# Performance work log

Measured on AMD Instinct MI355X. Metric: run time of the kernel, lower is better.

The kernel has to match this reference:

```python
import jax, jax.numpy as jnp
import numpy as np

N_NODES = 50000
N_EDGES = 800000
N_FEAT = 128
HIDDEN = 128
N_GRAPHS = 256


def gcn_conv(x, W, b, src, dst, n_nodes):
    # PyG GCNConv, add_self_loops=False, edge_weight=1:
    # out_i = sum_{(j->i)} d_j^{-1/2} d_i^{-1/2} (x_j @ W) + b, deg over target idx
    h = x @ W                                    # [N, out]
    deg = jax.ops.segment_sum(jnp.ones((src.shape[0],), h.dtype), dst,
                              num_segments=n_nodes)          # [N]
    dis = jnp.where(deg > 0, jax.lax.rsqrt(jnp.maximum(deg, 1.0)), 0.0)
    norm = dis[src] * dis[dst]                   # [E]
    msg = h[src] * norm[:, None]                 # [E, out] gather + scale
    out = jax.ops.segment_sum(msg, dst, num_segments=n_nodes)  # scatter-add
    return out + b


def setup_inputs() -> dict:
    key = jax.random.key(0)
    ks = jax.random.split(key, 12)
    x = jax.random.normal(ks[0], (N_NODES, N_FEAT), jnp.float32)
    edge_index = jax.random.randint(ks[1], (2, N_EDGES), 0, N_NODES, jnp.int64)
    batch = jnp.sort(jax.random.randint(ks[2], (N_NODES,), 0, N_GRAPHS, jnp.int64))

    def glorot(k, shape):
        lim = float(np.sqrt(6.0 / (shape[0] + shape[1])))
        return jax.random.uniform(k, shape, jnp.float32, -lim, lim)

    W1 = glorot(ks[3], (N_FEAT, HIDDEN)); b1 = jnp.zeros((HIDDEN,), jnp.float32)
    W2 = glorot(ks[4], (HIDDEN, HIDDEN)); b2 = jnp.zeros((HIDDEN,), jnp.float32)
    Wf1 = glorot(ks[5], (HIDDEN, HIDDEN // 2)); bf1 = jnp.zeros((HIDDEN // 2,), jnp.float32)
    Wl = glorot(ks[6], (HIDDEN // 2, 2)); bl = jnp.zeros((2,), jnp.float32)
    return {"x": x, "edge_index": edge_index, "batch": batch,
            "W1": W1, "b1": b1, "W2": W2, "b2": b2,
            "Wf1": Wf1, "bf1": bf1, "Wl": Wl, "bl": bl}


def reference(x, edge_index, batch, W1, b1, W2, b2, Wf1, bf1, Wl, bl):
    src, dst = edge_index[0], edge_index[1]
    h = jax.nn.relu(gcn_conv(x, W1, b1, src, dst, N_NODES))
    h = jax.nn.relu(gcn_conv(h, W2, b2, src, dst, N_NODES))
    h = gcn_conv(h, W2, b2, src, dst, N_NODES)   # conv2 applied a second time (same weights)
    # global_mean_pool over graphs
    sums = jax.ops.segment_sum(h, batch, num_segments=N_GRAPHS)      # [G, H]
    cnts = jax.ops.segment_sum(jnp.ones((h.shape[0],), h.dtype), batch,
                               num_segments=N_GRAPHS)                # [G]
    g = sums / jnp.maximum(cnts, 1.0)[:, None]
    g = jax.nn.relu(g @ Wf1 + bf1)
    logits = g @ Wl + bl
    return jax.nn.softmax(logits, axis=1)
```

## Files before the change

kernel.cpp:

```cpp
#include <hip/hip_runtime.h>
#include <hip/hip_bf16.h>

#define N_NODES 50000
#define N_EDGES 800000
#define NF 128
#define NG 256
#define CAP 64
#define NSEG 256
#define SEGE (N_EDGES / NSEG)
#define NPAD 50048
#define NPREPB 16

typedef unsigned short ushort_t;
typedef unsigned char uchar_t;
typedef __attribute__((ext_vector_type(8))) short bf16x8;
typedef __attribute__((ext_vector_type(4))) float f32x4;

__device__ __forceinline__ float b2f(ushort_t u) {
    union { unsigned i; float f; } x; x.i = ((unsigned)u) << 16; return x.f;
}
__device__ __forceinline__ ushort_t f2b(float f) {
    union { float f; unsigned i; } x; x.f = f;
    unsigned r = (x.i + 0x7fffu + ((x.i >> 16) & 1u)) >> 16;
    return (ushort_t)r;
}

__global__ __launch_bounds__(512) void k_seg_count(
        const int* __restrict__ dst, uchar_t* __restrict__ segcnt,
        float* __restrict__ gsum) {
    __shared__ unsigned int cntw[NPAD / 4];
    int tid = threadIdx.x;
    int b = blockIdx.x;
    if (b < 16) {
        ((float4*)gsum)[b * 512 + tid] = make_float4(0.f, 0.f, 0.f, 0.f);
    }
    for (int i = tid; i < NPAD / 4; i += 512) cntw[i] = 0;
    __syncthreads();
    const int* d0 = dst + b * SEGE;
    for (int e = tid; e < SEGE; e += 512) {
        int d = d0[e];
        atomicAdd(&cntw[d >> 2], 1u << ((d & 3) * 8));
    }
    __syncthreads();
    unsigned int* outw = (unsigned int*)(segcnt + (size_t)b * NPAD);
    for (int i = tid; i < NPAD / 4; i += 512) outw[i] = cntw[i];
}

__global__ void k_seg_scan(const uchar_t* __restrict__ segcnt,
                           uchar_t* __restrict__ segbase,
                           int* __restrict__ deg, float* __restrict__ dis) {
    int node = blockIdx.x * 256 + threadIdx.x;
    if (node >= N_NODES) return;
    int run = 0;
#pragma unroll 8
    for (int s = 0; s < NSEG; ++s) {
        size_t idx = (size_t)s * NPAD + node;
        int c = segcnt[idx];
        segbase[idx] = (uchar_t)min(run, 255);
        run += c;
    }
    deg[node] = min(run, CAP);
    dis[node] = (run > 0) ? rsqrtf((float)run) : 0.f;
}

__global__ __launch_bounds__(512) void k_seg_fill(
        const int* __restrict__ src, const int* __restrict__ dst,
        const uchar_t* __restrict__ segbase, ushort_t* __restrict__ csr_pad,
        const float* __restrict__ W1, const float* __restrict__ W2,
        ushort_t* __restrict__ W1h, ushort_t* __restrict__ W1l,
        ushort_t* __restrict__ W2h, ushort_t* __restrict__ W2l) {
    __shared__ unsigned int cntw[NPAD / 4];
    int tid = threadIdx.x;
    int b = blockIdx.x;
    if (b >= NSEG) {
        int base = (b - NSEG) * 2048 + tid * 4;
#pragma unroll
        for (int i = 0; i < 4; ++i) {
            int id = base + i;
            int which = id >> 14;
            int u = id & 16383;
            int k = u >> 7, c = u & 127;
            const float* W = which ? W2 : W1;
            ushort_t* Wh = which ? W2h : W1h;
            ushort_t* Wl = which ? W2l : W1l;
            float w = W[k * 128 + c];
            ushort_t hi = f2b(w);
            ushort_t lo = f2b(w - b2f(hi));
            Wh[c * 128 + k] = hi;
            Wl[c * 128 + k] = lo;
        }
        return;
    }
    for (int i = tid; i < NPAD / 4; i += 512) cntw[i] = 0;
    __syncthreads();
    const int* d0 = dst + b * SEGE;
    const int* s0 = src + b * SEGE;
    const uchar_t* brow = segbase + (size_t)b * NPAD;
    for (int e = tid; e < SEGE; e += 512) {
        int d = d0[e];
        int sh = (d & 3) * 8;
        unsigned old = atomicAdd(&cntw[d >> 2], 1u << sh);
        int pos = (old >> sh) & 0xFF;
        int slot = brow[d] + pos;
        if (slot < CAP) csr_pad[(size_t)d * CAP + slot] = (ushort_t)s0[e];
    }
}

__global__ __launch_bounds__(256) void k_gemm_mfma_f32(
        const float* __restrict__ Xf,
        const ushort_t* __restrict__ Wt_hi, const ushort_t* __restrict__ Wt_lo,
        const float* __restrict__ dis, ushort_t* __restrict__ Yb, int n) {
    __shared__ ushort_t Wlds[2][16384];
    int t = threadIdx.x;
    {
        const int4* gh = (const int4*)Wt_hi;
        const int4* gl = (const int4*)Wt_lo;
        int4* sh = (int4*)&Wlds[0][0];
        int4* sl = (int4*)&Wlds[1][0];
#pragma unroll
        for (int i = 0; i < 8; ++i) {
            int u = t + i * 256;
            int swz = u ^ ((u >> 4) & 7);
            sh[swz] = gh[u];
            sl[swz] = gl[u];
        }
    }
    __syncthreads();

    int wid = t >> 6;
    int l   = t & 63;
    int la  = l & 15;
    int kb  = l >> 4;
    int r0  = blockIdx.x * 64 + wid * 16;

    bf16x8 a[4];
    {
        int ra = min(r0 + la, n - 1);
        const float* xrow = Xf + (size_t)ra * 128 + kb * 8;
#pragma unroll
        for (int kt = 0; kt < 4; ++kt) {
            float4 v0 = *(const float4*)(xrow + kt * 32);
            float4 v1 = *(const float4*)(xrow + kt * 32 + 4);
            bf16x8 av;
            av[0] = (short)f2b(v0.x); av[1] = (short)f2b(v0.y);
            av[2] = (short)f2b(v0.z); av[3] = (short)f2b(v0.w);
            av[4] = (short)f2b(v1.x); av[5] = (short)f2b(v1.y);
            av[6] = (short)f2b(v1.z); av[7] = (short)f2b(v1.w);
            a[kt] = av;
        }
    }

    f32x4 acc[8];
#pragma unroll
    for (int ct = 0; ct < 8; ++ct) acc[ct] = (f32x4){0.f, 0.f, 0.f, 0.f};

#pragma unroll
    for (int ct = 0; ct < 8; ++ct) {
        int c = ct * 16 + la;
        int ubase = c * 128 + kb * 8;
        int sw = (c & 7) << 3;
#pragma unroll
        for (int kt = 0; kt < 4; ++kt) {
            int u16 = (ubase + kt * 32) ^ sw;
            bf16x8 bh = *(const bf16x8*)&Wlds[0][u16];
            bf16x8 bl = *(const bf16x8*)&Wlds[1][u16];
            acc[ct] = __builtin_amdgcn_mfma_f32_16x16x32_bf16(a[kt], bh, acc[ct], 0, 0, 0);
            acc[ct] = __builtin_amdgcn_mfma_f32_16x16x32_bf16(a[kt], bl, acc[ct], 0, 0, 0);
        }
    }

    float dsc[4];
#pragma unroll
    for (int j = 0; j < 4; ++j)
        dsc[j] = dis[min(r0 + kb * 4 + j, n - 1)];

    __syncthreads();
    ushort_t* tile = ((ushort_t*)Wlds) + wid * 2048;
#pragma unroll
    for (int ct = 0; ct < 8; ++ct) {
        int cc = ct * 16 + la;
#pragma unroll
        for (int j = 0; j < 4; ++j)
            tile[(kb * 4 + j) * 128 + cc] = f2b(acc[ct][j] * dsc[j]);
    }
    __syncthreads();
    {
        const int4* t4 = (const int4*)tile;
        int4* dst4 = (int4*)(Yb + (size_t)r0 * 128);
#pragma unroll
        for (int i = 0; i < 4; ++i) {
            int u = l * 4 + i;
            int row = u >> 4;
            if (r0 + row < n) dst4[u] = t4[u];
        }
    }
}

__global__ __launch_bounds__(256) void k_gemm_mfma_bf16(
        const ushort_t* __restrict__ Xb,
        const ushort_t* __restrict__ Wt_hi, const ushort_t* __restrict__ Wt_lo,
        const float* __restrict__ dis, ushort_t* __restrict__ Yb, int n) {
    __shared__ ushort_t Wlds[2][16384];
    int t = threadIdx.x;
    {
        const int4* gh = (const int4*)Wt_hi;
        const int4* gl = (const int4*)Wt_lo;
        int4* sh = (int4*)&Wlds[0][0];
        int4* sl = (int4*)&Wlds[1][0];
#pragma unroll
        for (int i = 0; i < 8; ++i) {
            int u = t + i * 256;
            int swz = u ^ ((u >> 4) & 7);
            sh[swz] = gh[u];
            sl[swz] = gl[u];
        }
    }
    __syncthreads();

    int wid = t >> 6;
    int l   = t & 63;
    int la  = l & 15;
    int kb  = l >> 4;
    int r0  = blockIdx.x * 64 + wid * 16;

    bf16x8 a[4];
    {
        int ra = min(r0 + la, n - 1);
        const ushort_t* xrow = Xb + (size_t)ra * 128 + kb * 8;
#pragma unroll
        for (int kt = 0; kt < 4; ++kt)
            a[kt] = *(const bf16x8*)(xrow + kt * 32);
    }

    f32x4 acc[8];
#pragma unroll
    for (int ct = 0; ct < 8; ++ct) acc[ct] = (f32x4){0.f, 0.f, 0.f, 0.f};

#pragma unroll
    for (int ct = 0; ct < 8; ++ct) {
        int c = ct * 16 + la;
        int ubase = c * 128 + kb * 8;
        int sw = (c & 7) << 3;
#pragma unroll
        for (int kt = 0; kt < 4; ++kt) {
            int u16 = (ubase + kt * 32) ^ sw;
            bf16x8 bh = *(const bf16x8*)&Wlds[0][u16];
            bf16x8 bl = *(const bf16x8*)&Wlds[1][u16];
            acc[ct] = __builtin_amdgcn_mfma_f32_16x16x32_bf16(a[kt], bh, acc[ct], 0, 0, 0);
            acc[ct] = __builtin_amdgcn_mfma_f32_16x16x32_bf16(a[kt], bl, acc[ct], 0, 0, 0);
        }
    }

    float dsc[4];
#pragma unroll
    for (int j = 0; j < 4; ++j)
        dsc[j] = dis[min(r0 + kb * 4 + j, n - 1)];

    __syncthreads();
    ushort_t* tile = ((ushort_t*)Wlds) + wid * 2048;
#pragma unroll
    for (int ct = 0; ct < 8; ++ct) {
        int cc = ct * 16 + la;
#pragma unroll
        for (int j = 0; j < 4; ++j)
            tile[(kb * 4 + j) * 128 + cc] = f2b(acc[ct][j] * dsc[j]);
    }
    __syncthreads();
    {
        const int4* t4 = (const int4*)tile;
        int4* dst4 = (int4*)(Yb + (size_t)r0 * 128);
#pragma unroll
        for (int i = 0; i < 4; ++i) {
            int u = l * 4 + i;
            int row = u >> 4;
            if (r0 + row < n) dst4[u] = t4[u];
        }
    }
}

template <bool RELU>
__global__ __launch_bounds__(256) void k_agg(
        const ushort_t* __restrict__ Hs, const int* __restrict__ deg,
        const ushort_t* __restrict__ csr_pad, const float* __restrict__ dis,
        const float* __restrict__ bias, ushort_t* __restrict__ out, int n) {
    int lane = threadIdx.x & 31;
    int sub  = threadIdx.x >> 5;
    int node = blockIdx.x * 8 + sub;
    if (node >= n) return;
    int dg = deg[node];
    const ushort_t* lst = csr_pad + (size_t)node * CAP;
    int c0 = lane * 4;

    float4 a0 = make_float4(0.f, 0.f, 0.f, 0.f);
    float4 a1 = make_float4(0.f, 0.f, 0.f, 0.f);
    float4 a2 = make_float4(0.f, 0.f, 0.f, 0.f);
    float4 a3 = make_float4(0.f, 0.f, 0.f, 0.f);
    float4 a4 = make_float4(0.f, 0.f, 0.f, 0.f);
    float4 a5 = make_float4(0.f, 0.f, 0.f, 0.f);
    float4 a6 = make_float4(0.f, 0.f, 0.f, 0.f);
    float4 a7 = make_float4(0.f, 0.f, 0.f, 0.f);
    int p = 0;
    for (; p + 7 < dg; p += 8) {
        int j0 = lst[p],     j1 = lst[p + 1], j2 = lst[p + 2], j3 = lst[p + 3];
        int j4 = lst[p + 4], j5 = lst[p + 5], j6 = lst[p + 6], j7 = lst[p + 7];
        ushort4 v0 = *(const ushort4*)&Hs[(size_t)j0 * 128 + c0];
        ushort4 v1 = *(const ushort4*)&Hs[(size_t)j1 * 128 + c0];
        ushort4 v2 = *(const ushort4*)&Hs[(size_t)j2 * 128 + c0];
        ushort4 v3 = *(const ushort4*)&Hs[(size_t)j3 * 128 + c0];
        ushort4 v4 = *(const ushort4*)&Hs[(size_t)j4 * 128 + c0];
        ushort4 v5 = *(const ushort4*)&Hs[(size_t)j5 * 128 + c0];
        ushort4 v6 = *(const ushort4*)&Hs[(size_t)j6 * 128 + c0];
        ushort4 v7 = *(const ushort4*)&Hs[(size_t)j7 * 128 + c0];
        a0.x += b2f(v0.x); a0.y += b2f(v0.y); a0.z += b2f(v0.z); a0.w += b2f(v0.w);
        a1.x += b2f(v1.x); a1.y += b2f(v1.y); a1.z += b2f(v1.z); a1.w += b2f(v1.w);
        a2.x += b2f(v2.x); a2.y += b2f(v2.y); a2.z += b2f(v2.z); a2.w += b2f(v2.w);
        a3.x += b2f(v3.x); a3.y += b2f(v3.y); a3.z += b2f(v3.z); a3.w += b2f(v3.w);
        a4.x += b2f(v4.x); a4.y += b2f(v4.y); a4.z += b2f(v4.z); a4.w += b2f(v4.w);
        a5.x += b2f(v5.x); a5.y += b2f(v5.y); a5.z += b2f(v5.z); a5.w += b2f(v5.w);
        a6.x += b2f(v6.x); a6.y += b2f(v6.y); a6.z += b2f(v6.z); a6.w += b2f(v6.w);
        a7.x += b2f(v7.x); a7.y += b2f(v7.y); a7.z += b2f(v7.z); a7.w += b2f(v7.w);
    }
    for (; p + 3 < dg; p += 4) {
        int j0 = lst[p], j1 = lst[p + 1], j2 = lst[p + 2], j3 = lst[p + 3];
        ushort4 v0 = *(const ushort4*)&Hs[(size_t)j0 * 128 + c0];
        ushort4 v1 = *(const ushort4*)&Hs[(size_t)j1 * 128 + c0];
        ushort4 v2 = *(const ushort4*)&Hs[(size_t)j2 * 128 + c0];
        ushort4 v3 = *(const ushort4*)&Hs[(size_t)j3 * 128 + c0];
        a0.x += b2f(v0.x); a0.y += b2f(v0.y); a0.z += b2f(v0.z); a0.w += b2f(v0.w);
        a1.x += b2f(v1.x); a1.y += b2f(v1.y); a1.z += b2f(v1.z); a1.w += b2f(v1.w);
        a2.x += b2f(v2.x); a2.y += b2f(v2.y); a2.z += b2f(v2.z); a2.w += b2f(v2.w);
        a3.x += b2f(v3.x); a3.y += b2f(v3.y); a3.z += b2f(v3.z); a3.w += b2f(v3.w);
    }
    for (; p < dg; ++p) {
        int j = lst[p];
        ushort4 v = *(const ushort4*)&Hs[(size_t)j * 128 + c0];
        a0.x += b2f(v.x); a0.y += b2f(v.y); a0.z += b2f(v.z); a0.w += b2f(v.w);
    }
    float dsc = dis[node];
    float4 b = *(const float4*)&bias[c0];
    float rx = (((a0.x + a1.x) + (a2.x + a3.x)) + ((a4.x + a5.x) + (a6.x + a7.x))) * dsc + b.x;
    float ry = (((a0.y + a1.y) + (a2.y + a3.y)) + ((a4.y + a5.y) + (a6.y + a7.y))) * dsc + b.y;
    float rz = (((a0.z + a1.z) + (a2.z + a3.z)) + ((a4.z + a5.z) + (a6.z + a7.z))) * dsc + b.z;
    float rw = (((a0.w + a1.w) + (a2.w + a3.w)) + ((a4.w + a5.w) + (a6.w + a7.w))) * dsc + b.w;
    if (RELU) {
        rx = fmaxf(rx, 0.f); ry = fmaxf(ry, 0.f);
        rz = fmaxf(rz, 0.f); rw = fmaxf(rw, 0.f);
    }
    ushort4 o;
    o.x = f2b(rx); o.y = f2b(ry); o.z = f2b(rz); o.w = f2b(rw);
    *(ushort4*)&out[(size_t)node * 128 + c0] = o;
}

#define POOL_CHUNK 128
__global__ __launch_bounds__(128) void k_pool_partial(
        const ushort_t* __restrict__ H, const int* __restrict__ batch,
        float* __restrict__ gsum, int n) {
    int f = threadIdx.x;
    int s = blockIdx.x * POOL_CHUNK;
    int e = min(s + POOL_CHUNK, n);
    if (s >= n) return;
    float acc = 0.f;
    int g = batch[s];
    for (int i = s; i < e; ++i) {
        int bg = batch[i];
        if (bg != g) {
            atomicAdd(&gsum[g * 128 + f], acc);
            acc = 0.f;
            g = bg;
        }
        acc += b2f(H[(size_t)i * 128 + f]);
    }
    atomicAdd(&gsum[g * 128 + f], acc);
}

__global__ void k_head(const float* __restrict__ gsum, const int* __restrict__ batch,
                       const float* __restrict__ Wf1, const float* __restrict__ bf1,
                       const float* __restrict__ Wl, const float* __restrict__ bl,
                       float* __restrict__ out, int n) {
    int g = blockIdx.x;
    int j = threadIdx.x;
    __shared__ float xs[128];
    __shared__ float hs[64];

    int lo = 0, hi = n;
    while (lo < hi) { int m = (lo + hi) >> 1; if (batch[m] < g) lo = m + 1; else hi = m; }
    int s0 = lo;
    hi = n;
    while (lo < hi) { int m = (lo + hi) >> 1; if (batch[m] <= g) lo = m + 1; else hi = m; }
    float inv_cnt = 1.f / fmaxf((float)(lo - s0), 1.f);

    xs[j]      = gsum[g * 128 + j] * inv_cnt;
    xs[j + 64] = gsum[g * 128 + 64 + j] * inv_cnt;
    __syncthreads();
    float acc = bf1[j];
#pragma unroll 4
    for (int k = 0; k < 128; k++) acc += xs[k] * Wf1[k * 64 + j];
    hs[j] = fmaxf(acc, 0.f);
    __syncthreads();
    if (j == 0) {
        float l0 = bl[0], l1 = bl[1];
        for (int k = 0; k < 64; k++) { l0 += hs[k] * Wl[k * 2 + 0]; l1 += hs[k] * Wl[k * 2 + 1]; }
        float m  = fmaxf(l0, l1);
        float e0 = expf(l0 - m), e1 = expf(l1 - m);
        float inv = 1.f / (e0 + e1);
        out[g * 2 + 0] = e0 * inv;
        out[g * 2 + 1] = e1 * inv;
    }
}

extern "C" void kernel_launch(void* const* d_in, const int* in_sizes, int n_in,
                              void* d_out, int out_size, void* d_ws, size_t ws_size,
                              hipStream_t stream) {
    const float* x    = (const float*)d_in[0];
    const int*   eidx = (const int*)d_in[1];
    const int*   batch= (const int*)d_in[2];
    const float* W1   = (const float*)d_in[3];
    const float* b1   = (const float*)d_in[4];
    const float* W2   = (const float*)d_in[5];
    const float* b2   = (const float*)d_in[6];
    const float* Wf1  = (const float*)d_in[7];
    const float* bf1  = (const float*)d_in[8];
    const float* Wl   = (const float*)d_in[9];
    const float* bl   = (const float*)d_in[10];
    float* out = (float*)d_out;

    const int* src = eidx;
    const int* dst = eidx + N_EDGES;

    char* w = (char*)d_ws;
    auto alloc = [&](size_t bytes) -> void* {
        void* p = (void*)w;
        w += (bytes + 255) & ~(size_t)255;
        return p;
    };
    ushort_t* Yb     = (ushort_t*)alloc((size_t)N_NODES * NF * 2);
    ushort_t* Hb     = (ushort_t*)alloc((size_t)N_NODES * NF * 2);
    ushort_t* W1h    = (ushort_t*)alloc((size_t)NF * NF * 2);
    ushort_t* W1l    = (ushort_t*)alloc((size_t)NF * NF * 2);
    ushort_t* W2h    = (ushort_t*)alloc((size_t)NF * NF * 2);
    ushort_t* W2l    = (ushort_t*)alloc((size_t)NF * NF * 2);
    float*    dis    = (float*)alloc((size_t)N_NODES * 4);
    int*      deg    = (int*)  alloc((size_t)N_NODES * 4);
    ushort_t* csr_pad= (ushort_t*)alloc((size_t)N_NODES * CAP * 2);
    uchar_t*  segcnt = (uchar_t*)alloc((size_t)NSEG * NPAD);
    uchar_t*  segbase= (uchar_t*)alloc((size_t)NSEG * NPAD);
    float*    gsum   = (float*)alloc((size_t)NG * NF * 4);

    k_seg_count<<<NSEG, 512, 0, stream>>>(dst, segcnt, gsum);
    k_seg_scan<<<(N_NODES + 255) / 256, 256, 0, stream>>>(segcnt, segbase, deg, dis);
    k_seg_fill<<<NSEG + NPREPB, 512, 0, stream>>>(src, dst, segbase, csr_pad,
                                                  W1, W2, W1h, W1l, W2h, W2l);

    int gb = (N_NODES + 63) / 64;
    int ab = (N_NODES + 7) / 8;
    k_gemm_mfma_f32<<<gb, 256, 0, stream>>>(x, W1h, W1l, dis, Yb, N_NODES);
    k_agg<true><<<ab, 256, 0, stream>>>(Yb, deg, csr_pad, dis, b1, Hb, N_NODES);
    k_gemm_mfma_bf16<<<gb, 256, 0, stream>>>(Hb, W2h, W2l, dis, Yb, N_NODES);
    k_agg<true><<<ab, 256, 0, stream>>>(Yb, deg, csr_pad, dis, b2, Hb, N_NODES);
    k_gemm_mfma_bf16<<<gb, 256, 0, stream>>>(Hb, W2h, W2l, dis, Yb, N_NODES);
    k_agg<false><<<ab, 256, 0, stream>>>(Yb, deg, csr_pad, dis, b2, Hb, N_NODES);

    k_pool_partial<<<(N_NODES + POOL_CHUNK - 1) / POOL_CHUNK, 128, 0, stream>>>(Hb, batch, gsum, N_NODES);
    k_head<<<NG, 64, 0, stream>>>(gsum, batch, Wf1, bf1, Wl, bl, out, N_NODES);
}
```

Before: 235.0 us.

## Merge CSR build and pool/head stages into cooperative kernels with grid sync

Replaces the three CSR-build launches (count, scan, fill) with one cooperative kernel that uses grid.sync between phases. It likewise merges the pooling and classifier head into one cooperative kernel. The aim is to remove kernel launch gaps and inter-kernel drain. The risks are the cost of grid-wide barriers and the scan phase running on only 256 blocks of 512 threads. Each block also holds about 50KB of LDS, which may limit residency for the cooperative launch.

Result: slower. 359.4 us (+52.9%).

```diff
diff --git a/kernel.cpp b/kernel.cpp
--- a/kernel.cpp
+++ b/kernel.cpp
@@ -1,5 +1,8 @@
 #include <hip/hip_runtime.h>
 #include <hip/hip_bf16.h>
+#include <hip/hip_cooperative_groups.h>
+
+namespace cg = cooperative_groups;
 
 #define N_NODES 50000
 #define N_EDGES 800000
@@ -9,7 +12,7 @@
 #define NSEG 256
 #define SEGE (N_EDGES / NSEG)
 #define NPAD 50048
-#define NPREPB 16
+#define NPOOLB ((N_NODES + 127) / 128)
 
 typedef unsigned short ushort_t;
 typedef unsigned char uchar_t;
@@ -25,58 +28,53 @@
     return (ushort_t)r;
 }
 
-__global__ __launch_bounds__(512) void k_seg_count(
-        const int* __restrict__ dst, uchar_t* __restrict__ segcnt,
-        float* __restrict__ gsum) {
-    __shared__ unsigned int cntw[NPAD / 4];
-    int tid = threadIdx.x;
-    int b = blockIdx.x;
-    if (b < 16) {
-        ((float4*)gsum)[b * 512 + tid] = make_float4(0.f, 0.f, 0.f, 0.f);
-    }
-    for (int i = tid; i < NPAD / 4; i += 512) cntw[i] = 0;
-    __syncthreads();
-    const int* d0 = dst + b * SEGE;
-    for (int e = tid; e < SEGE; e += 512) {
-        int d = d0[e];
-        atomicAdd(&cntw[d >> 2], 1u << ((d & 3) * 8));
-    }
-    __syncthreads();
-    unsigned int* outw = (unsigned int*)(segcnt + (size_t)b * NPAD);
-    for (int i = tid; i < NPAD / 4; i += 512) outw[i] = cntw[i];
-}
-
-__global__ void k_seg_scan(const uchar_t* __restrict__ segcnt,
-                           uchar_t* __restrict__ segbase,
-                           int* __restrict__ deg, float* __restrict__ dis) {
-    int node = blockIdx.x * 256 + threadIdx.x;
-    if (node >= N_NODES) return;
-    int run = 0;
-#pragma unroll 8
-    for (int s = 0; s < NSEG; ++s) {
-        size_t idx = (size_t)s * NPAD + node;
-        int c = segcnt[idx];
-        segbase[idx] = (uchar_t)min(run, 255);
-        run += c;
-    }
-    deg[node] = min(run, CAP);
-    dis[node] = (run > 0) ? rsqrtf((float)run) : 0.f;
-}
-
-__global__ __launch_bounds__(512) void k_seg_fill(
+__global__ __launch_bounds__(512) void k_build_coop(
         const int* __restrict__ src, const int* __restrict__ dst,
-        const uchar_t* __restrict__ segbase, ushort_t* __restrict__ csr_pad,
+        uchar_t* __restrict__ segcnt, uchar_t* __restrict__ segbase,
+        int* __restrict__ deg, float* __restrict__ dis,
+        ushort_t* __restrict__ csr_pad, float* __restrict__ gsum,
         const float* __restrict__ W1, const float* __restrict__ W2,
         ushort_t* __restrict__ W1h, ushort_t* __restrict__ W1l,
         ushort_t* __restrict__ W2h, ushort_t* __restrict__ W2l) {
     __shared__ unsigned int cntw[NPAD / 4];
+    cg::grid_group grid = cg::this_grid();
     int tid = threadIdx.x;
     int b = blockIdx.x;
-    if (b >= NSEG) {
-        int base = (b - NSEG) * 2048 + tid * 4;
-#pragma unroll
-        for (int i = 0; i < 4; ++i) {
-            int id = base + i;
+
+    if (b < 16) {
+        ((float4*)gsum)[b * 512 + tid] = make_float4(0.f, 0.f, 0.f, 0.f);
+    }
+    for (int i = tid; i < NPAD / 4; i += 512) cntw[i] = 0;
+    __syncthreads();
+    {
+        const int* d0 = dst + b * SEGE;
+        for (int e = tid; e < SEGE; e += 512) {
+            int d = d0[e];
+            atomicAdd(&cntw[d >> 2], 1u << ((d & 3) * 8));
+        }
+    }
+    __syncthreads();
+    {
+        unsigned int* outw = (unsigned int*)(segcnt + (size_t)b * NPAD);
+        for (int i = tid; i < NPAD / 4; i += 512) outw[i] = cntw[i];
+    }
+    grid.sync();
+
+    {
+        int gid = b * 512 + tid;
+        if (gid < N_NODES) {
+            int run = 0;
+#pragma unroll 8
+            for (int s = 0; s < NSEG; ++s) {
+                size_t idx = (size_t)s * NPAD + gid;
+                int c = segcnt[idx];
+                segbase[idx] = (uchar_t)min(run, 255);
+                run += c;
+            }
+            deg[gid] = min(run, CAP);
+            dis[gid] = (run > 0) ? rsqrtf((float)run) : 0.f;
+        } else if (gid < N_NODES + 2 * NF * NF) {
+            int id = gid - N_NODES;
             int which = id >> 14;
             int u = id & 16383;
             int k = u >> 7, c = u & 127;
@@ -89,20 +87,23 @@
             Wh[c * 128 + k] = hi;
             Wl[c * 128 + k] = lo;
         }
-        return;
-    }
+    }
+    grid.sync();
+
     for (int i = tid; i < NPAD / 4; i += 512) cntw[i] = 0;
     __syncthreads();
-    const int* d0 = dst + b * SEGE;
-    const int* s0 = src + b * SEGE;
-    const uchar_t* brow = segbase + (size_t)b * NPAD;
-    for (int e = tid; e < SEGE; e += 512) {
-        int d = d0[e];
-        int sh = (d & 3) * 8;
-        unsigned old = atomicAdd(&cntw[d >> 2], 1u << sh);
-        int pos = (old >> sh) & 0xFF;
-        int slot = brow[d] + pos;
-        if (slot < CAP) csr_pad[(size_t)d * CAP + slot] = (ushort_t)s0[e];
+    {
+        const int* d0 = dst + b * SEGE;
+        const int* s0 = src + b * SEGE;
+        const uchar_t* brow = segbase + (size_t)b * NPAD;
+        for (int e = tid; e < SEGE; e += 512) {
+            int d = d0[e];
+            int sh = (d & 3) * 8;
+            unsigned old = atomicAdd(&cntw[d >> 2], 1u << sh);
+            int pos = (old >> sh) & 0xFF;
+            int slot = brow[d] + pos;
+            if (slot < CAP) csr_pad[(size_t)d * CAP + slot] = (ushort_t)s0[e];
+        }
     }
 }
 
@@ -351,60 +352,63 @@
     *(ushort4*)&out[(size_t)node * 128 + c0] = o;
 }
 
-#define POOL_CHUNK 128
-__global__ __launch_bounds__(128) void k_pool_partial(
+__global__ __launch_bounds__(128) void k_pool_head(
         const ushort_t* __restrict__ H, const int* __restrict__ batch,
-        float* __restrict__ gsum, int n) {
-    int f = threadIdx.x;
-    int s = blockIdx.x * POOL_CHUNK;
-    int e = min(s + POOL_CHUNK, n);
-    if (s >= n) return;
-    float acc = 0.f;
-    int g = batch[s];
-    for (int i = s; i < e; ++i) {
-        int bg = batch[i];
-        if (bg != g) {
-            atomicAdd(&gsum[g * 128 + f], acc);
-            acc = 0.f;
-            g = bg;
-        }
-        acc += b2f(H[(size_t)i * 128 + f]);
-    }
-    atomicAdd(&gsum[g * 128 + f], acc);
-}
-
-__global__ void k_head(const float* __restrict__ gsum, const int* __restrict__ batch,
-                       const float* __restrict__ Wf1, const float* __restrict__ bf1,
-                       const float* __restrict__ Wl, const float* __restrict__ bl,
-                       float* __restrict__ out, int n) {
-    int g = blockIdx.x;
-    int j = threadIdx.x;
+        float* __restrict__ gsum, const float* __restrict__ Wf1,
+        const float* __restrict__ bf1, const float* __restrict__ Wl,
+        const float* __restrict__ bl, float* __restrict__ out, int n) {
     __shared__ float xs[128];
     __shared__ float hs[64];
-
-    int lo = 0, hi = n;
-    while (lo < hi) { int m = (lo + hi) >> 1; if (batch[m] < g) lo = m + 1; else hi = m; }
-    int s0 = lo;
-    hi = n;
-    while (lo < hi) { int m = (lo + hi) >> 1; if (batch[m] <= g) lo = m + 1; else hi = m; }
-    float inv_cnt = 1.f / fmaxf((float)(lo - s0), 1.f);
-
-    xs[j]      = gsum[g * 128 + j] * inv_cnt;
-    xs[j + 64] = gsum[g * 128 + 64 + j] * inv_cnt;
-    __syncthreads();
-    float acc = bf1[j];
+    cg::grid_group grid = cg::this_grid();
+    int j = threadIdx.x;
+
+    {
+        int s = blockIdx.x * 128;
+        int e = min(s + 128, n);
+        if (s < n) {
+            float acc = 0.f;
+            int g = batch[s];
+            for (int i = s; i < e; ++i) {
+                int bg = batch[i];
+                if (bg != g) {
+                    atomicAdd(&gsum[g * 128 + j], acc);
+                    acc = 0.f;
+                    g = bg;
+                }
+                acc += b2f(H[(size_t)i * 128 + j]);
+            }
+            atomicAdd(&gsum[g * 128 + j], acc);
+        }
+    }
+    grid.sync();
+
+    if (blockIdx.x < NG) {
+        int g = blockIdx.x;
+        int lo = 0, hi = n;
+        while (lo < hi) { int m = (lo + hi) >> 1; if (batch[m] < g) lo = m + 1; else hi = m; }
+        int s0 = lo;
+        hi = n;
+        while (lo < hi) { int m = (lo + hi) >> 1; if (batch[m] <= g) lo = m + 1; else hi = m; }
+        float inv_cnt = 1.f / fmaxf((float)(lo - s0), 1.f);
+
+        xs[j] = gsum[g * 128 + j] * inv_cnt;
+        __syncthreads();
+        if (j < 64) {
+            float acc = bf1[j];
 #pragma unroll 4
-    for (int k = 0; k < 128; k++) acc += xs[k] * Wf1[k * 64 + j];
-    hs[j] = fmaxf(acc, 0.f);
-    __syncthreads();
-    if (j == 0) {
-        float l0 = bl[0], l1 = bl[1];
-        for (int k = 0; k < 64; k++) { l0 += hs[k] * Wl[k * 2 + 0]; l1 += hs[k] * Wl[k * 2 + 1]; }
-        float m  = fmaxf(l0, l1);
-        float e0 = expf(l0 - m), e1 = expf(l1 - m);
-        float inv = 1.f / (e0 + e1);
-        out[g * 2 + 0] = e0 * inv;
-        out[g * 2 + 1] = e1 * inv;
+            for (int k = 0; k < 128; k++) acc += xs[k] * Wf1[k * 64 + j];
+            hs[j] = fmaxf(acc, 0.f);
+        }
+        __syncthreads();
+        if (j == 0) {
+            float l0 = bl[0], l1 = bl[1];
+            for (int k = 0; k < 64; k++) { l0 += hs[k] * Wl[k * 2 + 0]; l1 += hs[k] * Wl[k * 2 + 1]; }
+            float m  = fmaxf(l0, l1);
+            float e0 = expf(l0 - m), e1 = expf(l1 - m);
+            float inv = 1.f / (e0 + e1);
+            out[g * 2 + 0] = e0 * inv;
+            out[g * 2 + 1] = e1 * inv;
+        }
     }
 }
 
@@ -446,10 +450,14 @@
     uchar_t*  segbase= (uchar_t*)alloc((size_t)NSEG * NPAD);
     float*    gsum   = (float*)alloc((size_t)NG * NF * 4);
 
-    k_seg_count<<<NSEG, 512, 0, stream>>>(dst, segcnt, gsum);
-    k_seg_scan<<<(N_NODES + 255) / 256, 256, 0, stream>>>(segcnt, segbase, deg, dis);
-    k_seg_fill<<<NSEG + NPREPB, 512, 0, stream>>>(src, dst, segbase, csr_pad,
-                                                  W1, W2, W1h, W1l, W2h, W2l);
+    {
+        void* args[] = { (void*)&src, (void*)&dst, (void*)&segcnt, (void*)&segbase,
+                         (void*)&deg, (void*)&dis, (void*)&csr_pad, (void*)&gsum,
+                         (void*)&W1, (void*)&W2, (void*)&W1h, (void*)&W1l,
+                         (void*)&W2h, (void*)&W2l };
+        hipLaunchCooperativeKernel((void*)k_build_coop, dim3(NSEG), dim3(512),
+                                   args, 0, stream);
+    }
 
     int gb = (N_NODES + 63) / 64;
     int ab = (N_NODES + 7) / 8;
@@ -460,6 +468,11 @@
     k_gemm_mfma_bf16<<<gb, 256, 0, stream>>>(Hb, W2h, W2l, dis, Yb, N_NODES);
     k_agg<false><<<ab, 256, 0, stream>>>(Yb, deg, csr_pad, dis, b2, Hb, N_NODES);
 
-    k_pool_partial<<<(N_NODES + POOL_CHUNK - 1) / POOL_CHUNK, 128, 0, stream>>>(Hb, batch, gsum, N_NODES);
-    k_head<<<NG, 64, 0, stream>>>(gsum, batch, Wf1, bf1, Wl, bl, out, N_NODES);
-}
+    {
+        int n = N_NODES;
+        void* args[] = { (void*)&Hb, (void*)&batch, (void*)&gsum, (void*)&Wf1,
+                         (void*)&bf1, (void*)&Wl, (void*)&bl, (void*)&out, (void*)&n };
+        hipLaunchCooperativeKernel((void*)k_pool_head, dim3(NPOOLB), dim3(128),
+                                   args, 0, stream);
+    }
+}
```
